# Performance work log

Measured on AMD Instinct MI355X. Metric: run time of the kernel, lower is better.

Reference implementation:

```python
import jax, jax.numpy as jnp
import numpy as np

B, C, H, W = 4, 512, 64, 64
CK = C // 8  # key/query channels


def setup_inputs() -> dict:
    key = jax.random.key(0)
    ks = jax.random.split(key, 4)
    x = jax.random.normal(ks[0], (B, C, H, W), dtype=jnp.float32)
    # 1x1 conv weights -> plain [out, in] matrices; fan-in scaled like torch default-ish
    Wf = jax.random.normal(ks[1], (CK, C), dtype=jnp.float32) * (1.0 / np.sqrt(C))
    Wg = jax.random.normal(ks[2], (CK, C), dtype=jnp.float32) * (1.0 / np.sqrt(C))
    Wh = jax.random.normal(ks[3], (C, C), dtype=jnp.float32) * (1.0 / np.sqrt(C))
    bf = jnp.zeros((CK,), dtype=jnp.float32)
    bg = jnp.zeros((CK,), dtype=jnp.float32)
    bh = jnp.zeros((C,), dtype=jnp.float32)
    gamma = jnp.zeros((1,), dtype=jnp.float32)
    return {"x": x, "Wf": Wf, "bf": bf, "Wg": Wg, "bg": bg, "Wh": Wh, "bh": bh, "gamma": gamma}


def reference(x, Wf, bf, Wg, bg, Wh, bh, gamma):
    b, c, h, w = x.shape
    n = h * w
    xf = x.reshape(b, c, n)  # [B, C, N]
    # 1x1 convs == per-pixel linear maps
    f = jnp.einsum('kc,bcn->bkn', Wf, xf) + bf[None, :, None]  # [B, CK, N]
    g = jnp.einsum('kc,bcn->bkn', Wg, xf) + bg[None, :, None]  # [B, CK, N]
    hx = jnp.einsum('oc,bcn->bon', Wh, xf) + bh[None, :, None]  # [B, C, N]
    # energy[b,i,j] = sum_k f[b,k,i] * g[b,k,j]  (f_x.permute(0,2,1) @ g_x)
    energy = jnp.einsum('bki,bkj->bij', f, g)  # [B, N, N]
    attention = jax.nn.softmax(energy, axis=-1)
    # out[b,c,i] = sum_j hx[b,c,j] * attention[b,i,j]  (h_x @ attention^T)
    out = jnp.einsum('bcj,bij->bci', hx, attention)  # [B, C, N]
    out = out.reshape(b, c, h, w)
    return gamma[0] * out + x
```

## Files before the change

kernel.cpp:

```cpp
#include <hip/hip_runtime.h>
#include <hip/hip_bf16.h>

#define NB 4
#define CC 512
#define NN 4096
#define CKK 64

typedef _Float16 f16x4 __attribute__((ext_vector_type(4)));
typedef _Float16 f16x8 __attribute__((ext_vector_type(8)));
typedef float    f32x4 __attribute__((ext_vector_type(4)));

__device__ __forceinline__ void g2l16(const _Float16* g, _Float16* l) {
    __builtin_amdgcn_global_load_lds(
        (const __attribute__((address_space(1))) void*)g,
        (__attribute__((address_space(3))) void*)l, 16, 0, 0);
}

__device__ __forceinline__ void stage_tile(const _Float16* __restrict__ g, int ldg,
                                           _Float16* lds, int lane, int wave) {
    #pragma unroll
    for (int r = 0; r < 2; r++) {
        int q = r * 4 + wave;
        int row = q * 16 + (lane >> 2);
        int col = (lane & 3) * 8;
        g2l16(g + (size_t)row * ldg + col, lds + q * 512 + lane * 8);
    }
}

__launch_bounds__(256)
__global__ void transpose_x(const float* __restrict__ x, _Float16* __restrict__ xT) {
    const int N = NN, C = CC;
    int n0 = blockIdx.x * 64, c0 = blockIdx.y * 64, b = blockIdx.z;
    __shared__ float T[64][65];
    int t = threadIdx.x;
    const float* xb = x + (size_t)b * C * N;
    #pragma unroll
    for (int r = 0; r < 4; r++) {
        int c = (t >> 4) + 16 * r;
        int n4 = (t & 15) * 4;
        float4 v = *(const float4*)(xb + (size_t)(c0 + c) * N + n0 + n4);
        T[n4 + 0][c] = v.x; T[n4 + 1][c] = v.y; T[n4 + 2][c] = v.z; T[n4 + 3][c] = v.w;
    }
    __syncthreads();
    int n = t >> 2, cb = (t & 3) * 16;
    f16x8 h0, h1;
    #pragma unroll
    for (int i = 0; i < 8; i++) { h0[i] = (_Float16)T[n][cb + i]; h1[i] = (_Float16)T[n][cb + 8 + i]; }
    _Float16* dst = xT + (size_t)b * N * C + (size_t)(n0 + n) * C + c0 + cb;
    *(f16x8*)dst = h0;
    *(f16x8*)(dst + 8) = h1;
}

__launch_bounds__(256)
__global__ void convert_w(const float* __restrict__ Wf, const float* __restrict__ bf_,
                          const float* __restrict__ Wg, const float* __restrict__ bg_,
                          const float* __restrict__ Wh, const float* __restrict__ bh_,
                          _Float16* __restrict__ Wall, float* __restrict__ Ball) {
    int o = blockIdx.x;
    int t = threadIdx.x;
    const float* src;
    if (o < 64)       src = Wf + (size_t)o * CC;
    else if (o < 128) src = Wg + (size_t)(o - 64) * CC;
    else              src = Wh + (size_t)(o - 128) * CC;
    Wall[(size_t)o * CC + t]       = (_Float16)src[t];
    Wall[(size_t)o * CC + 256 + t] = (_Float16)src[256 + t];
    if (t == 0)
        Ball[o] = (o < 64) ? bf_[o] : (o < 128 ? bg_[o - 64] : bh_[o - 128]);
}

__launch_bounds__(256)
__global__ void proj_mfma(const _Float16* __restrict__ xT, const _Float16* __restrict__ Wall,
                          const float* __restrict__ Ball,
                          _Float16* __restrict__ Ft, _Float16* __restrict__ Gt,
                          _Float16* __restrict__ Hx) {
    const int N = NN, C = CC;
    int n0 = blockIdx.x * 128;
    int o0 = blockIdx.y * 128;
    int b  = blockIdx.z;
    const _Float16* Arow = Wall + (size_t)o0 * C;
    const _Float16* Brow = xT + (size_t)b * N * C + (size_t)n0 * C;
    __shared__ _Float16 As[128 * 32];
    __shared__ _Float16 Bs[128 * 32];
    int tid = threadIdx.x, lane = tid & 63, wave = tid >> 6;
    int wm = wave & 1, wn = wave >> 1, lrow = lane & 15, quad = lane >> 4;
    f32x4 acc[4][4] = {};
    for (int kc = 0; kc < C; kc += 32) {
        __syncthreads();
        stage_tile(Arow + kc, C, As, lane, wave);
        stage_tile(Brow + kc, C, Bs, lane, wave);
        __syncthreads();
        f16x8 af[4], bf[4];
        #pragma unroll
        for (int mi = 0; mi < 4; mi++)
            af[mi] = *(const f16x8*)(As + (wm * 64 + mi * 16 + lrow) * 32 + quad * 8);
        #pragma unroll
        for (int ni = 0; ni < 4; ni++)
            bf[ni] = *(const f16x8*)(Bs + (wn * 64 + ni * 16 + lrow) * 32 + quad * 8);
        #pragma unroll
        for (int mi = 0; mi < 4; mi++)
            #pragma unroll
            for (int ni = 0; ni < 4; ni++)
                acc[mi][ni] = __builtin_amdgcn_mfma_f32_16x16x32_f16(af[mi], bf[ni], acc[mi][ni], 0, 0, 0);
    }
    float bias_r[4][4];
    #pragma unroll
    for (int mi = 0; mi < 4; mi++)
        #pragma unroll
        for (int r = 0; r < 4; r++)
            bias_r[mi][r] = Ball[o0 + wm * 64 + mi * 16 + quad * 4 + r];
    _Float16* Ftb = Ft + (size_t)b * NN * CKK;
    _Float16* Gtb = Gt + (size_t)b * NN * CKK;
    _Float16* Hxb = Hx + (size_t)b * CC * N;
    #pragma unroll
    for (int mi = 0; mi < 4; mi++)
        #pragma unroll
        for (int ni = 0; ni < 4; ni++)
            #pragma unroll
            for (int r = 0; r < 4; r++) {
                int o = o0 + wm * 64 + mi * 16 + quad * 4 + r;
                int n = n0 + wn * 64 + ni * 16 + lrow;
                _Float16 v = (_Float16)(acc[mi][ni][r] + bias_r[mi][r]);
                if (o < 64)       Ftb[(size_t)n * CKK + o] = v;
                else if (o < 128) Gtb[(size_t)n * CKK + (o - 64)] = v;
                else              Hxb[(size_t)(o - 128) * N + n] = v;
            }
}

__launch_bounds__(256)
__global__ void energy_fused(const _Float16* __restrict__ Ft, const _Float16* __restrict__ Gt,
                             _Float16* __restrict__ P, float* __restrict__ Mpart,
                             float* __restrict__ Lpart, int r0, int Rstr) {
    const int N = NN;
    int b = blockIdx.z;
    const _Float16* Arow = Ft + (size_t)b * N * CKK + (size_t)(r0 + blockIdx.y * 128) * CKK;
    const _Float16* Brow = Gt + (size_t)b * N * CKK + (size_t)(blockIdx.x * 128) * CKK;
    _Float16* Pb = P + (size_t)b * Rstr * N + (size_t)blockIdx.y * 128 * N + blockIdx.x * 128;
    __shared__ _Float16 As[128 * 32];
    __shared__ _Float16 Bs[128 * 32];
    __shared__ float Sred[640];
    int tid = threadIdx.x, lane = tid & 63, wave = tid >> 6;
    int wm = wave & 1, wn = wave >> 1, lrow = lane & 15, quad = lane >> 4;
    f32x4 acc[4][4] = {};
    #pragma unroll
    for (int kc = 0; kc < CKK; kc += 32) {
        __syncthreads();
        stage_tile(Arow + kc, CKK, As, lane, wave);
        stage_tile(Brow + kc, CKK, Bs, lane, wave);
        __syncthreads();
        f16x8 af[4], bf[4];
        #pragma unroll
        for (int mi = 0; mi < 4; mi++)
            af[mi] = *(const f16x8*)(As + (wm * 64 + mi * 16 + lrow) * 32 + quad * 8);
        #pragma unroll
        for (int ni = 0; ni < 4; ni++)
            bf[ni] = *(const f16x8*)(Bs + (wn * 64 + ni * 16 + lrow) * 32 + quad * 8);
        #pragma unroll
        for (int mi = 0; mi < 4; mi++)
            #pragma unroll
            for (int ni = 0; ni < 4; ni++)
                acc[mi][ni] = __builtin_amdgcn_mfma_f32_16x16x32_f16(af[mi], bf[ni], acc[mi][ni], 0, 0, 0);
    }
    float mloc[16];
    #pragma unroll
    for (int mi = 0; mi < 4; mi++)
        #pragma unroll
        for (int r = 0; r < 4; r++) {
            float v = acc[mi][0][r];
            #pragma unroll
            for (int ni = 1; ni < 4; ni++) v = fmaxf(v, acc[mi][ni][r]);
            mloc[mi * 4 + r] = v;
        }
    #pragma unroll
    for (int off = 1; off < 16; off <<= 1)
        #pragma unroll
        for (int s = 0; s < 16; s++)
            mloc[s] = fmaxf(mloc[s], __shfl_xor(mloc[s], off));
    {
        float v = mloc[0];
        #pragma unroll
        for (int s = 1; s < 16; s++) v = (lrow == s) ? mloc[s] : v;
        int row = wm * 64 + (lrow >> 2) * 16 + quad * 4 + (lrow & 3);
        Sred[wn * 128 + row] = v;
    }
    __syncthreads();
    if (tid < 128) Sred[512 + tid] = fmaxf(Sred[tid], Sred[128 + tid]);
    __syncthreads();
    float lloc[16];
    #pragma unroll
    for (int mi = 0; mi < 4; mi++)
        #pragma unroll
        for (int r = 0; r < 4; r++) {
            int row = wm * 64 + mi * 16 + quad * 4 + r;
            float m = Sred[512 + row];
            float s = 0.f;
            #pragma unroll
            for (int ni = 0; ni < 4; ni++) {
                int j = wn * 64 + ni * 16 + lrow;
                float s16 = (float)(_Float16)acc[mi][ni][r];
                _Float16 p16 = (_Float16)__expf(s16 - m);
                Pb[(size_t)row * N + j] = p16;
                s += (float)p16;
            }
            lloc[mi * 4 + r] = s;
        }
    #pragma unroll
    for (int off = 1; off < 16; off <<= 1)
        #pragma unroll
        for (int s = 0; s < 16; s++)
            lloc[s] += __shfl_xor(lloc[s], off);
    {
        float v = lloc[0];
        #pragma unroll
        for (int s = 1; s < 16; s++) v = (lrow == s) ? lloc[s] : v;
        int row = wm * 64 + (lrow >> 2) * 16 + quad * 4 + (lrow & 3);
        Sred[256 + wn * 128 + row] = v;
    }
    __syncthreads();
    if (tid < 128) {
        size_t sidx = ((size_t)b * 32 + blockIdx.x) * Rstr + blockIdx.y * 128 + tid;
        Mpart[sidx] = Sred[512 + tid];
        Lpart[sidx] = Sred[256 + tid] + Sred[256 + 128 + tid];
    }
}

__launch_bounds__(256)
__global__ void combine_stats(const float* __restrict__ Mpart, const float* __restrict__ Lpart,
                              _Float16* __restrict__ cfac, int rows, int Rstr) {
    int b = blockIdx.y;
    int i = blockIdx.x * 256 + threadIdx.x;
    if (i >= rows) return;
    const float* mp = Mpart + (size_t)b * 32 * Rstr + i;
    const float* lp = Lpart + (size_t)b * 32 * Rstr + i;
    float m = -1e30f;
    #pragma unroll
    for (int jt = 0; jt < 32; jt++) m = fmaxf(m, mp[(size_t)jt * Rstr]);
    float l = 0.f;
    #pragma unroll
    for (int jt = 0; jt < 32; jt++)
        l += lp[(size_t)jt * Rstr] * __expf(mp[(size_t)jt * Rstr] - m);
    float linv = 1.0f / l;
    _Float16* cf = cfac + (size_t)b * 32 * Rstr + i;
    #pragma unroll
    for (int jt = 0; jt < 32; jt++)
        cf[(size_t)jt * Rstr] = (_Float16)(__expf(mp[(size_t)jt * Rstr] - m) * linv);
}

__launch_bounds__(256)
__global__ void out_mfma(const _Float16* __restrict__ Hx, const _Float16* __restrict__ P,
                         const _Float16* __restrict__ cfac,
                         const float* __restrict__ x, const float* __restrict__ gamma,
                         float* __restrict__ out, int r0, int Rstr) {
    const int N = NN, C = CC;
    int b = blockIdx.z;
    int i0l = blockIdx.x * 128;
    int c0  = blockIdx.y * 128;
    const _Float16* Arow = Hx + (size_t)b * C * N + (size_t)c0 * N;
    const _Float16* Brow = P  + (size_t)b * Rstr * N + (size_t)i0l * N;
    __shared__ _Float16 As[128 * 32];
    __shared__ _Float16 Bs[128 * 32];
    __shared__ _Float16 Cf[32 * 128];
    int tid = threadIdx.x, lane = tid & 63, wave = tid >> 6;
    int wm = wave & 1, wn = wave >> 1, lrow = lane & 15, quad = lane >> 4;
    #pragma unroll
    for (int r = 0; r < 16; r++) {
        int idx = tid + r * 256;
        int jt = idx >> 7, ii = idx & 127;
        Cf[idx] = cfac[((size_t)b * 32 + jt) * Rstr + i0l + ii];
    }
    __syncthreads();
    f32x4 acc[4][4] = {};
    for (int jt = 0; jt < 32; jt++) {
        _Float16 cfv[4];
        #pragma unroll
        for (int ni = 0; ni < 4; ni++)
            cfv[ni] = Cf[jt * 128 + wn * 64 + ni * 16 + lrow];
        #pragma unroll
        for (int kk = 0; kk < 4; kk++) {
            int kc = jt * 128 + kk * 32;
            __syncthreads();
            stage_tile(Arow + kc, N, As, lane, wave);
            stage_tile(Brow + kc, N, Bs, lane, wave);
            __syncthreads();
            f16x8 af[4], bf[4];
            #pragma unroll
            for (int mi = 0; mi < 4; mi++)
                af[mi] = *(const f16x8*)(As + (wm * 64 + mi * 16 + lrow) * 32 + quad * 8);
            #pragma unroll
            for (int ni = 0; ni < 4; ni++) {
                bf[ni] = *(const f16x8*)(Bs + (wn * 64 + ni * 16 + lrow) * 32 + quad * 8);
                #pragma unroll
                for (int j = 0; j < 8; j++) bf[ni][j] *= cfv[ni];
            }
            #pragma unroll
            for (int mi = 0; mi < 4; mi++)
                #pragma unroll
                for (int ni = 0; ni < 4; ni++)
                    acc[mi][ni] = __builtin_amdgcn_mfma_f32_16x16x32_f16(af[mi], bf[ni], acc[mi][ni], 0, 0, 0);
        }
    }
    float gv = gamma[0];
    const float* xb = x + (size_t)b * C * N;
    float* ob = out + (size_t)b * C * N;
    int ig0 = r0 + i0l;
    #pragma unroll
    for (int mi = 0; mi < 4; mi++)
        #pragma unroll
        for (int ni = 0; ni < 4; ni++)
            #pragma unroll
            for (int r = 0; r < 4; r++) {
                int c = c0 + wm * 64 + mi * 16 + quad * 4 + r;
                int i = ig0 + wn * 64 + ni * 16 + lrow;
                ob[(size_t)c * N + i] = gv * acc[mi][ni][r] + xb[(size_t)c * N + i];
            }
}

extern "C" void kernel_launch(void* const* d_in, const int* in_sizes, int n_in,
                              void* d_out, int out_size, void* d_ws, size_t ws_size,
                              hipStream_t stream) {
    const float* x     = (const float*)d_in[0];
    const float* Wf    = (const float*)d_in[1];
    const float* bf    = (const float*)d_in[2];
    const float* Wg    = (const float*)d_in[3];
    const float* bg    = (const float*)d_in[4];
    const float* Wh    = (const float*)d_in[5];
    const float* bh    = (const float*)d_in[6];
    const float* gamma = (const float*)d_in[7];
    float* out = (float*)d_out;

    const int B = NB, C = CC, N = NN;

    char* wsb = (char*)d_ws;
    _Float16* Wall = (_Float16*)wsb;
    float*    Ball = (float*)(wsb + ((size_t)768 << 10));
    _Float16* Ft = (_Float16*)(wsb + ((size_t)1 << 20));
    _Float16* Gt = (_Float16*)(wsb + ((size_t)3 << 20));
    _Float16* Hx = (_Float16*)(wsb + ((size_t)5 << 20));
    float* Mpart = (float*)(wsb + ((size_t)21 << 20));
    float* Lpart = (float*)(wsb + ((size_t)23 << 20));
    _Float16* cfac = (_Float16*)(wsb + ((size_t)25 << 20));
    _Float16* P  = (_Float16*)(wsb + ((size_t)26 << 20));
    _Float16* xT = P;
    size_t base = (size_t)26 << 20;
    size_t avail = (ws_size > base) ? ws_size - base : 0;
    size_t bytesPer128 = (size_t)B * N * 2 * 128;
    int R = (int)(avail / bytesPer128) * 128;
    if (R > N) R = N;
    if (R < 128) R = 128;

    transpose_x<<<dim3(N / 64, C / 64, B), dim3(256), 0, stream>>>(x, xT);
    convert_w<<<dim3(640), dim3(256), 0, stream>>>(Wf, bf, Wg, bg, Wh, bh, Wall, Ball);
    proj_mfma<<<dim3(N / 128, 5, B), dim3(256), 0, stream>>>(xT, Wall, Ball, Ft, Gt, Hx);

    for (int r0 = 0; r0 < N; r0 += R) {
        int rows = (R < N - r0) ? R : (N - r0);
        energy_fused<<<dim3(N / 128, rows / 128, B), dim3(256), 0, stream>>>(
            Ft, Gt, P, Mpart, Lpart, r0, R);
        combine_stats<<<dim3((rows + 255) / 256, B), dim3(256), 0, stream>>>(
            Mpart, Lpart, cfac, rows, R);
        out_mfma<<<dim3(rows / 128, C / 128, B), dim3(256), 0, stream>>>(
            Hx, P, cfac, x, gamma, out, r0, R);
    }
}
```

Baseline: 271.3 us.

## Stage P tile in LDS for coalesced stores, merge prep kernels, reorder out grid

The energy kernel now writes its exp'd probability tile into a padded LDS buffer and then stores it to global memory as 16-byte vectors. Before, each lane wrote a scattered 2-byte element. The transpose and weight-conversion kernels are merged into a single launch. The out_mfma grid is swapped so that blocks sharing a P row tile launch next to each other, which should improve L2 reuse of P. The LDS staging adds about 34KB of shared memory per block in energy_fused, which may lower occupancy.

```diff
diff --git a/kernel.cpp b/kernel.cpp
--- a/kernel.cpp
+++ b/kernel.cpp
@@ -28,44 +28,46 @@
 }
 
 __launch_bounds__(256)
-__global__ void transpose_x(const float* __restrict__ x, _Float16* __restrict__ xT) {
+__global__ void prep(const float* __restrict__ x, _Float16* __restrict__ xT,
+                     const float* __restrict__ Wf, const float* __restrict__ bf_,
+                     const float* __restrict__ Wg, const float* __restrict__ bg_,
+                     const float* __restrict__ Wh, const float* __restrict__ bh_,
+                     _Float16* __restrict__ Wall, float* __restrict__ Ball) {
     const int N = NN, C = CC;
-    int n0 = blockIdx.x * 64, c0 = blockIdx.y * 64, b = blockIdx.z;
-    __shared__ float T[64][65];
+    int bid = blockIdx.x;
     int t = threadIdx.x;
-    const float* xb = x + (size_t)b * C * N;
-    #pragma unroll
-    for (int r = 0; r < 4; r++) {
-        int c = (t >> 4) + 16 * r;
-        int n4 = (t & 15) * 4;
-        float4 v = *(const float4*)(xb + (size_t)(c0 + c) * N + n0 + n4);
-        T[n4 + 0][c] = v.x; T[n4 + 1][c] = v.y; T[n4 + 2][c] = v.z; T[n4 + 3][c] = v.w;
-    }
-    __syncthreads();
-    int n = t >> 2, cb = (t & 3) * 16;
-    f16x8 h0, h1;
-    #pragma unroll
-    for (int i = 0; i < 8; i++) { h0[i] = (_Float16)T[n][cb + i]; h1[i] = (_Float16)T[n][cb + 8 + i]; }
-    _Float16* dst = xT + (size_t)b * N * C + (size_t)(n0 + n) * C + c0 + cb;
-    *(f16x8*)dst = h0;
-    *(f16x8*)(dst + 8) = h1;
-}
-
-__launch_bounds__(256)
-__global__ void convert_w(const float* __restrict__ Wf, const float* __restrict__ bf_,
-                          const float* __restrict__ Wg, const float* __restrict__ bg_,
-                          const float* __restrict__ Wh, const float* __restrict__ bh_,
-                          _Float16* __restrict__ Wall, float* __restrict__ Ball) {
-    int o = blockIdx.x;
-    int t = threadIdx.x;
-    const float* src;
-    if (o < 64)       src = Wf + (size_t)o * CC;
-    else if (o < 128) src = Wg + (size_t)(o - 64) * CC;
-    else              src = Wh + (size_t)(o - 128) * CC;
-    Wall[(size_t)o * CC + t]       = (_Float16)src[t];
-    Wall[(size_t)o * CC + 256 + t] = (_Float16)src[256 + t];
-    if (t == 0)
-        Ball[o] = (o < 64) ? bf_[o] : (o < 128 ? bg_[o - 64] : bh_[o - 128]);
+    if (bid < 2048) {
+        int n0 = (bid & 63) << 6;
+        int c0 = ((bid >> 6) & 7) << 6;
+        int b  = bid >> 9;
+        __shared__ float T[64][65];
+        const float* xb = x + (size_t)b * C * N;
+        #pragma unroll
+        for (int r = 0; r < 4; r++) {
+            int c = (t >> 4) + 16 * r;
+            int n4 = (t & 15) * 4;
+            float4 v = *(const float4*)(xb + (size_t)(c0 + c) * N + n0 + n4);
+            T[n4 + 0][c] = v.x; T[n4 + 1][c] = v.y; T[n4 + 2][c] = v.z; T[n4 + 3][c] = v.w;
+        }
+        __syncthreads();
+        int n = t >> 2, cb = (t & 3) * 16;
+        f16x8 h0, h1;
+        #pragma unroll
+        for (int i = 0; i < 8; i++) { h0[i] = (_Float16)T[n][cb + i]; h1[i] = (_Float16)T[n][cb + 8 + i]; }
+        _Float16* dst = xT + (size_t)b * N * C + (size_t)(n0 + n) * C + c0 + cb;
+        *(f16x8*)dst = h0;
+        *(f16x8*)(dst + 8) = h1;
+    } else {
+        int o = bid - 2048;
+        const float* src;
+        if (o < 64)       src = Wf + (size_t)o * C;
+        else if (o < 128) src = Wg + (size_t)(o - 64) * C;
+        else              src = Wh + (size_t)(o - 128) * C;
+        Wall[(size_t)o * C + t]       = (_Float16)src[t];
+        Wall[(size_t)o * C + 256 + t] = (_Float16)src[256 + t];
+        if (t == 0)
+            Ball[o] = (o < 64) ? bf_[o] : (o < 128 ? bg_[o - 64] : bh_[o - 128]);
+    }
 }
 
 __launch_bounds__(256)
@@ -126,6 +128,7 @@
             }
 }
 
+#define PST_LD 136
 __launch_bounds__(256)
 __global__ void energy_fused(const _Float16* __restrict__ Ft, const _Float16* __restrict__ Gt,
                              _Float16* __restrict__ P, float* __restrict__ Mpart,
@@ -137,6 +140,7 @@
     _Float16* Pb = P + (size_t)b * Rstr * N + (size_t)blockIdx.y * 128 * N + blockIdx.x * 128;
     __shared__ _Float16 As[128 * 32];
     __shared__ _Float16 Bs[128 * 32];
+    __shared__ _Float16 Pst[128 * PST_LD];
     __shared__ float Sred[640];
     int tid = threadIdx.x, lane = tid & 63, wave = tid >> 6;
     int wm = wave & 1, wn = wave >> 1, lrow = lane & 15, quad = lane >> 4;
@@ -198,7 +202,7 @@
                 int j = wn * 64 + ni * 16 + lrow;
                 float s16 = (float)(_Float16)acc[mi][ni][r];
                 _Float16 p16 = (_Float16)__expf(s16 - m);
-                Pb[(size_t)row * N + j] = p16;
+                Pst[row * PST_LD + j] = p16;
                 s += (float)p16;
             }
             lloc[mi * 4 + r] = s;
@@ -220,6 +224,13 @@
         size_t sidx = ((size_t)b * 32 + blockIdx.x) * Rstr + blockIdx.y * 128 + tid;
         Mpart[sidx] = Sred[512 + tid];
         Lpart[sidx] = Sred[256 + tid] + Sred[256 + 128 + tid];
+    }
+    int col16 = tid & 15, rowb = tid >> 4;
+    #pragma unroll
+    for (int s = 0; s < 8; s++) {
+        int row = rowb + s * 16;
+        f16x8 v = *(const f16x8*)(Pst + row * PST_LD + col16 * 8);
+        *(f16x8*)(Pb + (size_t)row * N + col16 * 8) = v;
     }
 }
 
@@ -252,8 +263,8 @@
                          float* __restrict__ out, int r0, int Rstr) {
     const int N = NN, C = CC;
     int b = blockIdx.z;
-    int i0l = blockIdx.x * 128;
-    int c0  = blockIdx.y * 128;
+    int c0  = blockIdx.x * 128;
+    int i0l = blockIdx.y * 128;
     const _Float16* Arow = Hx + (size_t)b * C * N + (size_t)c0 * N;
     const _Float16* Brow = P  + (size_t)b * Rstr * N + (size_t)i0l * N;
     __shared__ _Float16 As[128 * 32];
@@ -347,8 +358,8 @@
     if (R > N) R = N;
     if (R < 128) R = 128;
 
-    transpose_x<<<dim3(N / 64, C / 64, B), dim3(256), 0, stream>>>(x, xT);
-    convert_w<<<dim3(640), dim3(256), 0, stream>>>(Wf, bf, Wg, bg, Wh, bh, Wall, Ball);
+    prep<<<dim3(2048 + 640), dim3(256), 0, stream>>>(
+        x, xT, Wf, bf, Wg, bg, Wh, bh, Wall, Ball);
     proj_mfma<<<dim3(N / 128, 5, B), dim3(256), 0, stream>>>(xT, Wall, Ball, Ft, Gt, Hx);
 
     for (int r0 = 0; r0 < N; r0 += R) {
@@ -357,7 +368,7 @@
             Ft, Gt, P, Mpart, Lpart, r0, R);
         combine_stats<<<dim3((rows + 255) / 256, B), dim3(256), 0, stream>>>(
             Mpart, Lpart, cfac, rows, R);
-        out_mfma<<<dim3(rows / 128, C / 128, B), dim3(256), 0, stream>>>(
+        out_mfma<<<dim3(C / 128, rows / 128, B), dim3(256), 0, stream>>>(
             Hx, P, cfac, x, gamma, out, r0, R);
     }
 }
```

After: 336.3 us. 24.0% more time.
